# Optimization experiments

Hardware: AMD Instinct MI355X
Metric: run time of the kernel (lower is better)

## Reference

```python
import jax, jax.numpy as jnp
import numpy as np

B, Q, K = 4, 128, 1024
DQ, DK, DV, H = 512, 512, 512, 256
NEG_INF = -1e6


def setup_inputs() -> dict:
    key = jax.random.key(0)
    ks = jax.random.split(key, 6)
    queries = jax.random.normal(ks[0], (B, Q, DQ), dtype=jnp.float32)
    keys = jax.random.normal(ks[1], (B, K, DK), dtype=jnp.float32)
    values = jax.random.normal(ks[2], (B, K, DV), dtype=jnp.float32)
    valid_lens = jax.random.randint(ks[3], (B,), 1, K + 1, dtype=jnp.int32)
    # Learned params (Dense use_bias=False): W_q [DQ,H], W_k [DK,H], w_v [H] (Dense(1) squeezed)
    Wq = jax.random.normal(ks[4], (DQ, H), dtype=jnp.float32) / np.sqrt(DQ)
    Wk = jax.random.normal(ks[5], (DK, H), dtype=jnp.float32) / np.sqrt(DK)
    wv = jax.random.normal(jax.random.fold_in(key, 7), (H,), dtype=jnp.float32) / np.sqrt(H)
    return {"queries": queries, "keys": keys, "values": values,
            "valid_lens": valid_lens, "Wq": Wq, "Wk": Wk, "wv": wv}


def reference(queries, keys, values, valid_lens, Wq, Wk, wv):
    q = queries @ Wq                       # [B,Q,H]
    k = keys @ Wk                          # [B,K,H]
    feats = jnp.tanh(q[:, :, None, :] + k[:, None, :, :])   # [B,Q,K,H]
    scores = jnp.einsum('bqkh,h->bqk', feats, wv)            # [B,Q,K]
    mask = jnp.arange(scores.shape[-1]) < valid_lens[:, None, None]  # [B,1,K]
    scores = jnp.where(mask, scores, NEG_INF)
    attn = jax.nn.softmax(scores, axis=-1)                   # [B,Q,K]
    # dropout is identity at inference
    return attn @ values                                     # [B,Q,DV]
```

## Files before the change

kernel.cpp:

```cpp
#include <hip/hip_runtime.h>

#define Bn 4
#define Qn 128
#define Kn 1024
#define Dn 512
#define Hn 256
#define SCALE 2.8853900817779268f
#define LOG2E 1.4426950408889634f

typedef __attribute__((ext_vector_type(8))) short short8;
typedef __attribute__((ext_vector_type(4))) float floatx4;

__device__ __forceinline__ unsigned short f2bf(float x) {
    unsigned int u = __float_as_uint(x);
    return (unsigned short)((u + 0x7fffu + ((u >> 16) & 1u)) >> 16);
}

__global__ __launch_bounds__(256) void prep_kernel(
    const float* __restrict__ queries, const float* __restrict__ keys,
    const float* __restrict__ Wq, const float* __restrict__ Wk,
    unsigned short* __restrict__ qk16,
    unsigned short* __restrict__ wtq, unsigned short* __restrict__ wtk)
{
    const int blk = blockIdx.x;
    const int t = threadIdx.x;
    if (blk < 64) {
        __shared__ float s_t[64][68];
        const int wsel = blk >> 5;
        const int tile = blk & 31;
        const int r0 = (tile >> 2) * 64;
        const int c0 = (tile & 3) * 64;
        const float* W = wsel ? Wk : Wq;
        unsigned short* Wt = wsel ? wtk : wtq;
        #pragma unroll
        for (int i = 0; i < 4; ++i) {
            int idx = t + i * 256;
            int row = idx >> 4, c4 = idx & 15;
            float4 v = *(const float4*)(W + (size_t)(r0 + row) * Hn + c0 + c4 * 4);
            s_t[row][c4*4+0] = v.x; s_t[row][c4*4+1] = v.y;
            s_t[row][c4*4+2] = v.z; s_t[row][c4*4+3] = v.w;
        }
        __syncthreads();
        const int n = c0 + (t >> 2);
        const int seg = t & 3;
        unsigned short tmp[16];
        #pragma unroll
        for (int i = 0; i < 16; ++i)
            tmp[i] = f2bf(s_t[seg * 16 + i][t >> 2]);
        uint4* dst = (uint4*)(Wt + (size_t)n * Dn + r0 + seg * 16);
        dst[0] = ((uint4*)tmp)[0];
        dst[1] = ((uint4*)tmp)[1];
    } else {
        const int cblk = blk - 64;
        const float* src = (cblk < 64) ? (queries + (size_t)cblk * 4096)
                                       : (keys + (size_t)(cblk - 64) * 4096);
        const float* s = src + t * 16;
        unsigned short tmp[16];
        #pragma unroll
        for (int i = 0; i < 4; ++i) {
            float4 v = *(const float4*)(s + i * 4);
            tmp[i*4+0] = f2bf(v.x); tmp[i*4+1] = f2bf(v.y);
            tmp[i*4+2] = f2bf(v.z); tmp[i*4+3] = f2bf(v.w);
        }
        uint4* dst = (uint4*)(qk16 + (size_t)cblk * 4096 + t * 16);
        dst[0] = ((uint4*)tmp)[0];
        dst[1] = ((uint4*)tmp)[1];
    }
}

__global__ __launch_bounds__(256) void proj_mfma_kernel(
    const unsigned short* __restrict__ qk16,
    const unsigned short* __restrict__ wtq,
    const unsigned short* __restrict__ wtk,
    const int* __restrict__ valid_lens,
    float* __restrict__ qproj, float* __restrict__ kproj)
{
    const int blk = blockIdx.x;
    const int nt = blk & 3;
    const int mt = blk >> 2;
    const int n0 = nt * 64;
    int arow0, drow0; const unsigned short* Wt; float* Dst;
    if (mt < 8) {
        arow0 = mt * 64; drow0 = arow0; Wt = wtq; Dst = qproj;
    } else {
        int r0 = (mt - 8) * 64;
        if ((r0 & 1023) >= valid_lens[r0 >> 10]) return;
        arow0 = 512 + r0; drow0 = r0; Wt = wtk; Dst = kproj;
    }
    const int t = threadIdx.x;
    const int lane = t & 63;
    const int w = t >> 6;

    __shared__ short8 s_a[512];
    __shared__ short8 s_b[512];

    int arow[2], brow[2], acol[2];
    #pragma unroll
    for (int i = 0; i < 2; ++i) {
        int s = t + i * 256;
        int grp = s >> 6, l = s & 63;
        int top = grp >> 1, kc = grp & 1;
        arow[i] = arow0 + top * 16 + (l & 15);
        brow[i] = n0 + top * 16 + (l & 15);
        acol[i] = kc * 32 + ((l >> 4) << 3);
    }

    floatx4 z = {0.f, 0.f, 0.f, 0.f};
    floatx4 acc0 = z, acc1 = z, acc2 = z, acc3 = z;

    for (int kt = 0; kt < 8; ++kt) {
        __syncthreads();
        #pragma unroll
        for (int i = 0; i < 2; ++i) {
            s_a[t + i*256] = *(const short8*)(qk16 + (size_t)arow[i] * Dn + kt*64 + acol[i]);
            s_b[t + i*256] = *(const short8*)(Wt   + (size_t)brow[i] * Dn + kt*64 + acol[i]);
        }
        __syncthreads();
        #pragma unroll
        for (int kc = 0; kc < 2; ++kc) {
            short8 a  = s_a[(w*2 + kc)*64 + lane];
            short8 b0 = s_b[(0  + kc)*64 + lane];
            short8 b1 = s_b[(2  + kc)*64 + lane];
            short8 b2 = s_b[(4  + kc)*64 + lane];
            short8 b3 = s_b[(6  + kc)*64 + lane];
            acc0 = __builtin_amdgcn_mfma_f32_16x16x32_bf16(a, b0, acc0, 0, 0, 0);
            acc1 = __builtin_amdgcn_mfma_f32_16x16x32_bf16(a, b1, acc1, 0, 0, 0);
            acc2 = __builtin_amdgcn_mfma_f32_16x16x32_bf16(a, b2, acc2, 0, 0, 0);
            acc3 = __builtin_amdgcn_mfma_f32_16x16x32_bf16(a, b3, acc3, 0, 0, 0);
        }
    }

    const int mrow = drow0 + w * 16 + ((lane >> 4) << 2);
    const int ncol = n0 + (lane & 15);
    float* dp = Dst + (size_t)mrow * Hn + ncol;
    floatx4 av[4] = {acc0, acc1, acc2, acc3};
    #pragma unroll
    for (int g = 0; g < 4; ++g)
        #pragma unroll
        for (int r = 0; r < 4; ++r)
            dp[(size_t)r * Hn + g * 16] = av[g][r] * SCALE;
}

__global__ __launch_bounds__(256) void score_kernel(
    const float* __restrict__ qproj, const float* __restrict__ kproj,
    const float* __restrict__ wv, const int* __restrict__ valid_lens,
    float* __restrict__ escores, float* __restrict__ rowsum)
{
    const int blk = blockIdx.x;
    const int kt = blk & 15;
    const int qt = (blk >> 4) & 7;
    const int b  = blk >> 7;
    const int vlen = valid_lens[b];
    const int k0 = kt * 64;
    if (k0 >= vlen) return;
    const int t = threadIdx.x;
    const int wave = __builtin_amdgcn_readfirstlane(t >> 6);
    const int lane = t & 63;

    __shared__ float s_kT[128][64];

    const float* qb = qproj + (size_t)(b * Qn + qt * 16 + wave * 4) * Hn;
    float acc2[4] = {0.f, 0.f, 0.f, 0.f};
    float sumw = 0.f;

    for (int ph = 0; ph < 2; ++ph) {
        __syncthreads();
        #pragma unroll
        for (int i = 0; i < 8; ++i) {
            int idx = t + i * 256;
            int k = idx & 63, h4 = idx >> 6;
            size_t off = (size_t)(b * Kn + k0 + k) * Hn + ph * 128 + h4 * 4;
            float4 p0 = *(const float4*)(kproj + off);
            s_kT[h4 * 4 + 0][k] = p0.x;
            s_kT[h4 * 4 + 1][k] = p0.y;
            s_kT[h4 * 4 + 2][k] = p0.z;
            s_kT[h4 * 4 + 3][k] = p0.w;
        }
        __syncthreads();
        #pragma unroll 4
        for (int h = 0; h < 128; ++h) {
            const int hg = ph * 128 + h;
            const float kv = s_kT[h][lane];
            const float wvh = wv[hg];
            const float q0 = qb[0 * Hn + hg];
            const float q1 = qb[1 * Hn + hg];
            const float q2 = qb[2 * Hn + hg];
            const float q3 = qb[3 * Hn + hg];
            sumw += wvh;
            float r0 = __builtin_amdgcn_rcpf(1.f + exp2f(q0 + kv));
            float r1 = __builtin_amdgcn_rcpf(1.f + exp2f(q1 + kv));
            float r2 = __builtin_amdgcn_rcpf(1.f + exp2f(q2 + kv));
            float r3 = __builtin_amdgcn_rcpf(1.f + exp2f(q3 + kv));
            acc2[0] = fmaf(wvh, r0, acc2[0]);
            acc2[1] = fmaf(wvh, r1, acc2[1]);
            acc2[2] = fmaf(wvh, r2, acc2[2]);
            acc2[3] = fmaf(wvh, r3, acc2[3]);
        }
    }

    const int k = k0 + lane;
    #pragma unroll
    for (int j = 0; j < 4; ++j) {
        float s = sumw - 2.f * acc2[j];
        float e = (k < vlen) ? exp2f(s * LOG2E) : 0.f;
        if (k < vlen)
            escores[(size_t)(b * Qn + qt * 16 + wave * 4 + j) * Kn + k] = e;
        #pragma unroll
        for (int off = 32; off; off >>= 1)
            e += __shfl_xor(e, off, 64);
        if (lane == 0)
            atomicAdd(&rowsum[b * Qn + qt * 16 + wave * 4 + j], e);
    }
}

__global__ __launch_bounds__(256) void av_kernel(
    const float* __restrict__ escores, const float* __restrict__ values,
    float* __restrict__ parts)
{
    const int blk = blockIdx.x;
    const int kc = blk & 3;
    const int dh = (blk >> 2) & 1;
    const int qt = (blk >> 3) & 15;
    const int b  = blk >> 7;
    const int t = threadIdx.x;
    const int q0 = qt * 8, kb = kc * 256, d = dh * 256 + t;

    const int ebase = __builtin_amdgcn_readfirstlane((b * Qn + q0) * Kn + kb);
    const float* vb = values + ((size_t)b * Kn + kb) * Dn + d;

    float acc[8] = {0.f, 0.f, 0.f, 0.f, 0.f, 0.f, 0.f, 0.f};
    #pragma unroll 2
    for (int k = 0; k < 256; k += 4) {
        float v0 = vb[(size_t)(k + 0) * Dn];
        float v1 = vb[(size_t)(k + 1) * Dn];
        float v2 = vb[(size_t)(k + 2) * Dn];
        float v3 = vb[(size_t)(k + 3) * Dn];
        #pragma unroll
        for (int j = 0; j < 8; ++j) {
            float4 e4 = *(const float4*)(escores + ebase + j * Kn + k);
            acc[j] += e4.x * v0 + e4.y * v1 + e4.z * v2 + e4.w * v3;
        }
    }
    float* pp = parts + (size_t)kc * (Bn * Qn * Dn) + (size_t)(b * Qn + q0) * Dn + d;
    #pragma unroll
    for (int j = 0; j < 8; ++j)
        pp[(size_t)j * Dn] = acc[j];
}

__global__ __launch_bounds__(256) void reduce_kernel(
    const float* __restrict__ parts, const float* __restrict__ rowsum,
    float* __restrict__ out)
{
    const int idx = blockIdx.x * 256 + threadIdx.x;
    const int row = (idx * 4) >> 9;
    const float inv = __builtin_amdgcn_rcpf(rowsum[row]);
    const float4* p = (const float4*)parts;
    float4 a = p[idx];
    float4 b = p[idx + 65536];
    float4 c = p[idx + 131072];
    float4 d = p[idx + 196608];
    float4 o;
    o.x = (a.x + b.x + c.x + d.x) * inv;
    o.y = (a.y + b.y + c.y + d.y) * inv;
    o.z = (a.z + b.z + c.z + d.z) * inv;
    o.w = (a.w + b.w + c.w + d.w) * inv;
    ((float4*)out)[idx] = o;
}

extern "C" void kernel_launch(void* const* d_in, const int* in_sizes, int n_in,
                              void* d_out, int out_size, void* d_ws, size_t ws_size,
                              hipStream_t stream) {
    const float* queries    = (const float*)d_in[0];
    const float* keys       = (const float*)d_in[1];
    const float* values     = (const float*)d_in[2];
    const int*   valid_lens = (const int*)  d_in[3];
    const float* Wq         = (const float*)d_in[4];
    const float* Wk         = (const float*)d_in[5];
    const float* wv         = (const float*)d_in[6];
    float* out = (float*)d_out;

    float* qproj   = (float*)d_ws;
    float* kproj   = qproj + Bn * Qn * Hn;
    float* escores = kproj + Bn * Kn * Hn;
    float* rowsum  = escores + Bn * Qn * Kn;
    float* parts   = rowsum + Bn * Qn;
    unsigned short* qk16 = (unsigned short*)(parts + 4 * Bn * Qn * Dn);
    unsigned short* wtq  = qk16 + 4608 * 512;
    unsigned short* wtk  = wtq + 256 * 512;

    hipMemsetAsync(escores, 0, (size_t)(Bn * Qn * Kn + Bn * Qn) * sizeof(float),
                   stream);
    prep_kernel<<<640, 256, 0, stream>>>(queries, keys, Wq, Wk, qk16, wtq, wtk);
    proj_mfma_kernel<<<288, 256, 0, stream>>>(qk16, wtq, wtk, valid_lens,
                                              qproj, kproj);
    score_kernel<<<512, 256, 0, stream>>>(qproj, kproj, wv, valid_lens,
                                          escores, rowsum);
    av_kernel<<<512, 256, 0, stream>>>(escores, values, parts);
    reduce_kernel<<<256, 256, 0, stream>>>(parts, rowsum, out);
}
```

Measured before the change: 176.2 us.

## Store projected keys transposed and drop LDS staging in score kernel

The projection kernel now writes the key projection in a transposed [B,H,K] layout, going through an LDS transpose so global stores stay coalesced. The score kernel reads keys straight from global memory with coalesced per-h loads instead of staging them in LDS. It also computes one query row per wave rather than four, with 4x more blocks. This removes shared-memory staging and barriers and raises parallelism, but each key value is now reused across fewer queries, so more global/L2 traffic and more redundant q and wv loads.

```diff
diff --git a/kernel.cpp b/kernel.cpp
--- a/kernel.cpp
+++ b/kernel.cpp
@@ -73,26 +73,27 @@
     const unsigned short* __restrict__ wtq,
     const unsigned short* __restrict__ wtk,
     const int* __restrict__ valid_lens,
-    float* __restrict__ qproj, float* __restrict__ kproj)
+    float* __restrict__ qproj, float* __restrict__ kprojT)
 {
     const int blk = blockIdx.x;
     const int nt = blk & 3;
     const int mt = blk >> 2;
     const int n0 = nt * 64;
-    int arow0, drow0; const unsigned short* Wt; float* Dst;
+    int arow0, drow0; const unsigned short* Wt; bool is_q;
     if (mt < 8) {
-        arow0 = mt * 64; drow0 = arow0; Wt = wtq; Dst = qproj;
+        arow0 = mt * 64; drow0 = arow0; Wt = wtq; is_q = true;
     } else {
         int r0 = (mt - 8) * 64;
         if ((r0 & 1023) >= valid_lens[r0 >> 10]) return;
-        arow0 = 512 + r0; drow0 = r0; Wt = wtk; Dst = kproj;
+        arow0 = 512 + r0; drow0 = r0; Wt = wtk; is_q = false;
     }
     const int t = threadIdx.x;
     const int lane = t & 63;
     const int w = t >> 6;
 
-    __shared__ short8 s_a[512];
-    __shared__ short8 s_b[512];
+    __shared__ float s_x[64 * 68];
+    short8* s_a = (short8*)s_x;
+    short8* s_b = (short8*)(s_x + 2048);
 
     int arow[2], brow[2], acol[2];
     #pragma unroll
@@ -130,87 +131,84 @@
         }
     }
 
-    const int mrow = drow0 + w * 16 + ((lane >> 4) << 2);
-    const int ncol = n0 + (lane & 15);
-    float* dp = Dst + (size_t)mrow * Hn + ncol;
     floatx4 av[4] = {acc0, acc1, acc2, acc3};
-    #pragma unroll
-    for (int g = 0; g < 4; ++g)
-        #pragma unroll
-        for (int r = 0; r < 4; ++r)
-            dp[(size_t)r * Hn + g * 16] = av[g][r] * SCALE;
+    if (is_q) {
+        const int mrow = drow0 + w * 16 + ((lane >> 4) << 2);
+        const int ncol = n0 + (lane & 15);
+        float* dp = qproj + (size_t)mrow * Hn + ncol;
+        #pragma unroll
+        for (int g = 0; g < 4; ++g)
+            #pragma unroll
+            for (int r = 0; r < 4; ++r)
+                dp[(size_t)r * Hn + g * 16] = av[g][r] * SCALE;
+    } else {
+        __syncthreads();
+        #pragma unroll
+        for (int g = 0; g < 4; ++g) {
+            const int n_loc = g * 16 + (lane & 15);
+            const int m_base = w * 16 + ((lane >> 4) << 2);
+            #pragma unroll
+            for (int r = 0; r < 4; ++r)
+                s_x[n_loc * 68 + m_base + r] = av[g][r] * SCALE;
+        }
+        __syncthreads();
+        const int bq = drow0 >> 10;
+        const int kk0 = drow0 & 1023;
+        float* dstT = kprojT + ((size_t)bq * Hn + n0) * Kn + kk0;
+        #pragma unroll
+        for (int i = 0; i < 4; ++i) {
+            int f4 = t + i * 256;
+            int row = f4 >> 4, c4 = f4 & 15;
+            *(float4*)(dstT + (size_t)row * Kn + c4 * 4) =
+                *(const float4*)&s_x[row * 68 + c4 * 4];
+        }
+    }
 }
 
 __global__ __launch_bounds__(256) void score_kernel(
-    const float* __restrict__ qproj, const float* __restrict__ kproj,
+    const float* __restrict__ qproj, const float* __restrict__ kprojT,
     const float* __restrict__ wv, const int* __restrict__ valid_lens,
     float* __restrict__ escores, float* __restrict__ rowsum)
 {
     const int blk = blockIdx.x;
     const int kt = blk & 15;
-    const int qt = (blk >> 4) & 7;
-    const int b  = blk >> 7;
+    const int qt = (blk >> 4) & 31;
+    const int b  = blk >> 9;
     const int vlen = valid_lens[b];
     const int k0 = kt * 64;
     if (k0 >= vlen) return;
     const int t = threadIdx.x;
     const int wave = __builtin_amdgcn_readfirstlane(t >> 6);
     const int lane = t & 63;
-
-    __shared__ float s_kT[128][64];
-
-    const float* qb = qproj + (size_t)(b * Qn + qt * 16 + wave * 4) * Hn;
-    float acc2[4] = {0.f, 0.f, 0.f, 0.f};
-    float sumw = 0.f;
-
-    for (int ph = 0; ph < 2; ++ph) {
-        __syncthreads();
-        #pragma unroll
-        for (int i = 0; i < 8; ++i) {
-            int idx = t + i * 256;
-            int k = idx & 63, h4 = idx >> 6;
-            size_t off = (size_t)(b * Kn + k0 + k) * Hn + ph * 128 + h4 * 4;
-            float4 p0 = *(const float4*)(kproj + off);
-            s_kT[h4 * 4 + 0][k] = p0.x;
-            s_kT[h4 * 4 + 1][k] = p0.y;
-            s_kT[h4 * 4 + 2][k] = p0.z;
-            s_kT[h4 * 4 + 3][k] = p0.w;
-        }
-        __syncthreads();
-        #pragma unroll 4
-        for (int h = 0; h < 128; ++h) {
-            const int hg = ph * 128 + h;
-            const float kv = s_kT[h][lane];
-            const float wvh = wv[hg];
-            const float q0 = qb[0 * Hn + hg];
-            const float q1 = qb[1 * Hn + hg];
-            const float q2 = qb[2 * Hn + hg];
-            const float q3 = qb[3 * Hn + hg];
-            sumw += wvh;
-            float r0 = __builtin_amdgcn_rcpf(1.f + exp2f(q0 + kv));
-            float r1 = __builtin_amdgcn_rcpf(1.f + exp2f(q1 + kv));
-            float r2 = __builtin_amdgcn_rcpf(1.f + exp2f(q2 + kv));
-            float r3 = __builtin_amdgcn_rcpf(1.f + exp2f(q3 + kv));
-            acc2[0] = fmaf(wvh, r0, acc2[0]);
-            acc2[1] = fmaf(wvh, r1, acc2[1]);
-            acc2[2] = fmaf(wvh, r2, acc2[2]);
-            acc2[3] = fmaf(wvh, r3, acc2[3]);
-        }
-    }
+    const int qrow = qt * 4 + wave;
+
+    const float* qb = qproj + (size_t)(b * Qn + qrow) * Hn;
+    const float* kb = kprojT + (size_t)b * Hn * Kn + k0 + lane;
+
+    float sumw = wv[lane] + wv[lane + 64] + wv[lane + 128] + wv[lane + 192];
+    #pragma unroll
+    for (int off = 32; off; off >>= 1)
+        sumw += __shfl_xor(sumw, off, 64);
+
+    float acc = 0.f;
+    #pragma unroll 8
+    for (int h = 0; h < Hn; ++h) {
+        float kv = kb[(size_t)h * Kn];
+        float qv = qb[h];
+        float wvh = wv[h];
+        acc = fmaf(wvh, __builtin_amdgcn_rcpf(1.f + exp2f(qv + kv)), acc);
+    }
+    float s = sumw - 2.f * acc;
 
     const int k = k0 + lane;
-    #pragma unroll
-    for (int j = 0; j < 4; ++j) {
-        float s = sumw - 2.f * acc2[j];
-        float e = (k < vlen) ? exp2f(s * LOG2E) : 0.f;
-        if (k < vlen)
-            escores[(size_t)(b * Qn + qt * 16 + wave * 4 + j) * Kn + k] = e;
-        #pragma unroll
-        for (int off = 32; off; off >>= 1)
-            e += __shfl_xor(e, off, 64);
-        if (lane == 0)
-            atomicAdd(&rowsum[b * Qn + qt * 16 + wave * 4 + j], e);
-    }
+    float e = (k < vlen) ? exp2f(s * LOG2E) : 0.f;
+    if (k < vlen)
+        escores[(size_t)(b * Qn + qrow) * Kn + k] = e;
+    #pragma unroll
+    for (int off = 32; off; off >>= 1)
+        e += __shfl_xor(e, off, 64);
+    if (lane == 0)
+        atomicAdd(&rowsum[b * Qn + qrow], e);
 }
 
 __global__ __launch_bounds__(256) void av_kernel(
@@ -280,8 +278,8 @@
     float* out = (float*)d_out;
 
     float* qproj   = (float*)d_ws;
-    float* kproj   = qproj + Bn * Qn * Hn;
-    float* escores = kproj + Bn * Kn * Hn;
+    float* kprojT  = qproj + Bn * Qn * Hn;
+    float* escores = kprojT + Bn * Hn * Kn;
     float* rowsum  = escores + Bn * Qn * Kn;
     float* parts   = rowsum + Bn * Qn;
     unsigned short* qk16 = (unsigned short*)(parts + 4 * Bn * Qn * Dn);
@@ -292,9 +290,9 @@
                    stream);
     prep_kernel<<<640, 256, 0, stream>>>(queries, keys, Wq, Wk, qk16, wtq, wtk);
     proj_mfma_kernel<<<288, 256, 0, stream>>>(qk16, wtq, wtk, valid_lens,
-                                              qproj, kproj);
-    score_kernel<<<512, 256, 0, stream>>>(qproj, kproj, wv, valid_lens,
-                                          escores, rowsum);
+                                              qproj, kprojT);
+    score_kernel<<<2048, 256, 0, stream>>>(qproj, kprojT, wv, valid_lens,
+                                           escores, rowsum);
     av_kernel<<<512, 256, 0, stream>>>(escores, values, parts);
     reduce_kernel<<<256, 256, 0, stream>>>(parts, rowsum, out);
 }
```

New measurement: 174.4 us. About the same (-1.0%).
